# Performance work log

Measured on AMD Instinct MI355X. Metric: run time of the kernel, lower is better.

The kernel has to match this reference:

```python
import jax, jax.numpy as jnp
import numpy as np
import math

H = 256
N = 100000

def setup_inputs() -> dict:
    key = jax.random.key(0)
    ks = jax.random.split(key, 8)
    def xavier(k, shape):
        fan_in, fan_out = shape
        bound = math.sqrt(6.0 / (fan_in + fan_out))
        return jax.random.uniform(k, shape, jnp.float32, -bound, bound)
    return {
        "x": jax.random.normal(ks[0], (N, H), jnp.float32),
        "vec": jax.random.normal(ks[1], (N, 3, H), jnp.float32),
        "node_frame": jax.random.normal(ks[2], (N, 3, 3), jnp.float32),
        # weights stored [in, out]
        "W_equi": xavier(ks[3], (H, 2 * H)),
        "W1": xavier(ks[4], (2 * H, H)),
        "b1": jnp.zeros((H,), jnp.float32),
        "W2": xavier(ks[5], (H, 3 * H)),
        "b2": jnp.zeros((3 * H,), jnp.float32),
    }

def reference(x, vec, node_frame, W_equi, W1, b1, W2, b2):
    inv_sqrt_2 = 1.0 / math.sqrt(2.0)
    inv_sqrt_h = 1.0 / math.sqrt(H)
    # equivariant projection: [N,3,H] @ [H,2H] -> [N,3,2H]
    v = jnp.einsum('nch,hk->nck', vec, W_equi)
    vec1, vec2 = v[..., :H], v[..., H:]
    # scalarization (dead in original output path; scalar below is what is used)
    scalar = jnp.linalg.norm(vec1, axis=-2)          # [N,H], norm over spatial dim
    vec_dot = jnp.sum(vec1 * vec2, axis=1) * inv_sqrt_h  # [N,H]
    h = jnp.concatenate([x, scalar], axis=-1)        # [N,2H]
    h = jax.nn.silu(h @ W1 + b1)                     # [N,H]
    x_vec_h = h @ W2 + b2                            # [N,3H]
    xvec1, xvec2, xvec3 = x_vec_h[:, :H], x_vec_h[:, H:2*H], x_vec_h[:, 2*H:]
    dx = (xvec1 + xvec2 + vec_dot) * inv_sqrt_2      # [N,H]
    dvec = xvec3[:, None, :] * vec2                  # [N,3,H]
    return (dx, dvec)
```

## Files before the change

kernel.cpp:

```cpp
#include <hip/hip_runtime.h>
#include <math.h>

#define H 256
#define R 4

__global__ __launch_bounds__(256) void fte_kernel(
    const float* __restrict__ x,
    const float* __restrict__ vec,
    const float* __restrict__ W_equi,
    const float* __restrict__ W1,
    const float* __restrict__ b1,
    const float* __restrict__ W2,
    const float* __restrict__ b2,
    float* __restrict__ dx,
    float* __restrict__ dvec,
    int N)
{
    __shared__ float vec_s[3 * R * H];
    __shared__ float v1_s[3 * R * H];
    __shared__ float v2_s[3 * R * H];
    __shared__ float hin_s[R * 2 * H];
    __shared__ float h_s[R * H];

    const int t = threadIdx.x;
    const int row0 = blockIdx.x * R;

    {
        const int valid = (N - row0) < R ? (N - row0) : R;
        const int total = valid * 3 * H;
        const float* src = vec + (size_t)row0 * 3 * H;
        if (total == 3 * R * H) {
            const float4* s4 = (const float4*)src;
            float4* d4 = (float4*)vec_s;
            #pragma unroll
            for (int i = 0; i < 3; ++i) d4[t + 256 * i] = s4[t + 256 * i];
        } else {
            for (int i = t; i < total; i += 256) vec_s[i] = src[i];
            for (int i = total + t; i < 3 * R * H; i += 256) vec_s[i] = 0.f;
        }
    }
    __syncthreads();

    float acc0[3 * R], acc1[3 * R];
    #pragma unroll
    for (int m = 0; m < 3 * R; ++m) { acc0[m] = 0.f; acc1[m] = 0.f; }
    for (int h = 0; h < H; h += 4) {
        float w0[4], w1[4];
        #pragma unroll
        for (int u = 0; u < 4; ++u) {
            const float2 w = *(const float2*)&W_equi[(size_t)(h + u) * 2 * H + 2 * t];
            w0[u] = w.x;
            w1[u] = w.y;
        }
        #pragma unroll
        for (int m = 0; m < 3 * R; ++m) {
            const float4 a = *(const float4*)&vec_s[m * H + h];
            acc0[m] += a.x * w0[0]; acc1[m] += a.x * w1[0];
            acc0[m] += a.y * w0[1]; acc1[m] += a.y * w1[1];
            acc0[m] += a.z * w0[2]; acc1[m] += a.z * w1[2];
            acc0[m] += a.w * w0[3]; acc1[m] += a.w * w1[3];
        }
    }
    {
        float* dst = (t < 128) ? v1_s : v2_s;
        const int kk = (2 * t) & (H - 1);
        #pragma unroll
        for (int m = 0; m < 3 * R; ++m) {
            float2 p; p.x = acc0[m]; p.y = acc1[m];
            *(float2*)&dst[m * H + kk] = p;
        }
    }
    __syncthreads();

    float vd[R];
    #pragma unroll
    for (int r = 0; r < R; ++r) {
        float s = 0.f, d = 0.f;
        #pragma unroll
        for (int c = 0; c < 3; ++c) {
            const float a = v1_s[(r * 3 + c) * H + t];
            const float b = v2_s[(r * 3 + c) * H + t];
            s += a * a;
            d += a * b;
        }
        vd[r] = d * (1.0f / 16.0f);
        hin_s[r * 2 * H + H + t] = sqrtf(s);
        float xv = 0.f;
        if (row0 + r < N) xv = x[(size_t)(row0 + r) * H + t];
        hin_s[r * 2 * H + t] = xv;
    }
    __syncthreads();

    float acc2[R];
    #pragma unroll
    for (int r = 0; r < R; ++r) acc2[r] = 0.f;
    for (int k = 0; k < 2 * H; k += 4) {
        float w[4];
        #pragma unroll
        for (int u = 0; u < 4; ++u) w[u] = W1[(size_t)(k + u) * H + t];
        #pragma unroll
        for (int r = 0; r < R; ++r) {
            const float4 a = *(const float4*)&hin_s[r * 2 * H + k];
            acc2[r] += a.x * w[0];
            acc2[r] += a.y * w[1];
            acc2[r] += a.z * w[2];
            acc2[r] += a.w * w[3];
        }
    }
    {
        const float bv = b1[t];
        #pragma unroll
        for (int r = 0; r < R; ++r) {
            const float z = acc2[r] + bv;
            h_s[r * H + t] = z / (1.f + __expf(-z));
        }
    }
    __syncthreads();

    float a3[R][3];
    #pragma unroll
    for (int r = 0; r < R; ++r)
        #pragma unroll
        for (int c = 0; c < 3; ++c) a3[r][c] = 0.f;
    for (int k = 0; k < H; k += 4) {
        float wc[4][3];
        #pragma unroll
        for (int u = 0; u < 4; ++u) {
            const float* wr = W2 + (size_t)(k + u) * 3 * H + t;
            wc[u][0] = wr[0];
            wc[u][1] = wr[H];
            wc[u][2] = wr[2 * H];
        }
        #pragma unroll
        for (int r = 0; r < R; ++r) {
            const float4 a = *(const float4*)&h_s[r * H + k];
            #pragma unroll
            for (int c = 0; c < 3; ++c) {
                a3[r][c] += a.x * wc[0][c];
                a3[r][c] += a.y * wc[1][c];
                a3[r][c] += a.z * wc[2][c];
                a3[r][c] += a.w * wc[3][c];
            }
        }
    }

    const float bv0 = b2[t];
    const float bv1 = b2[H + t];
    const float bv2 = b2[2 * H + t];
    const float inv_sqrt2 = 0.70710678118654752440f;
    #pragma unroll
    for (int r = 0; r < R; ++r) {
        const int n = row0 + r;
        if (n >= N) break;
        const float xv1 = a3[r][0] + bv0;
        const float xv2 = a3[r][1] + bv1;
        const float xv3 = a3[r][2] + bv2;
        dx[(size_t)n * H + t] = (xv1 + xv2 + vd[r]) * inv_sqrt2;
        #pragma unroll
        for (int c = 0; c < 3; ++c) {
            dvec[(size_t)n * 3 * H + c * H + t] = xv3 * v2_s[(r * 3 + c) * H + t];
        }
    }
}

extern "C" void kernel_launch(void* const* d_in, const int* in_sizes, int n_in,
                              void* d_out, int out_size, void* d_ws, size_t ws_size,
                              hipStream_t stream) {
    const float* x      = (const float*)d_in[0];
    const float* vec    = (const float*)d_in[1];
    const float* W_equi = (const float*)d_in[3];
    const float* W1     = (const float*)d_in[4];
    const float* b1     = (const float*)d_in[5];
    const float* W2     = (const float*)d_in[6];
    const float* b2     = (const float*)d_in[7];

    const int N = in_sizes[0] / H;
    float* dx   = (float*)d_out;
    float* dvec = (float*)d_out + (size_t)N * H;

    const int blocks = (N + R - 1) / R;
    fte_kernel<<<blocks, 256, 0, stream>>>(x, vec, W_equi, W1, b1, W2, b2, dx, dvec, N);
}
```

Before: 3.110 ms.

## Process 8 rows per block split into two thread groups with register-resident projections

Doubles rows per block to 8 and splits the 256 threads into two groups of 128, each handling 4 rows and two output columns per thread, so every weight load feeds more FMAs. The equivariant projection results stay in registers for the norm, dot product and dvec output instead of round-tripping through shared memory. A single reused shared buffer replaces the five separate arrays, and outputs use nontemporal stores. The cost is higher register pressure (launch bounds request 4 blocks per SM) and fewer blocks in the grid.

New measurement: 2.538 ms. -18.4%, faster.

```diff
diff --git a/kernel.cpp b/kernel.cpp
--- a/kernel.cpp
+++ b/kernel.cpp
@@ -2,9 +2,12 @@
 #include <math.h>
 
 #define H 256
-#define R 4
-
-__global__ __launch_bounds__(256) void fte_kernel(
+#define R 8
+#define RG 4
+#define AM (3*R)
+#define AMG (3*RG)
+
+__global__ __launch_bounds__(256, 4) void fte_kernel(
     const float* __restrict__ x,
     const float* __restrict__ vec,
     const float* __restrict__ W_equi,
@@ -16,149 +19,190 @@
     float* __restrict__ dvec,
     int N)
 {
-    __shared__ float vec_s[3 * R * H];
-    __shared__ float v1_s[3 * R * H];
-    __shared__ float v2_s[3 * R * H];
-    __shared__ float hin_s[R * 2 * H];
-    __shared__ float h_s[R * H];
-
-    const int t = threadIdx.x;
+    __shared__ float smem[AM * H];
+
+    const int t  = threadIdx.x;
+    const int g  = t >> 7;
+    const int tl = t & 127;
     const int row0 = blockIdx.x * R;
 
     {
-        const int valid = (N - row0) < R ? (N - row0) : R;
-        const int total = valid * 3 * H;
+        const int rem  = N - row0;
+        const int rows = rem < R ? rem : R;
+        const int total = rows * 3 * H;
         const float* src = vec + (size_t)row0 * 3 * H;
-        if (total == 3 * R * H) {
+        if (total == AM * H) {
             const float4* s4 = (const float4*)src;
-            float4* d4 = (float4*)vec_s;
-            #pragma unroll
-            for (int i = 0; i < 3; ++i) d4[t + 256 * i] = s4[t + 256 * i];
+            float4* d4 = (float4*)smem;
+            #pragma unroll
+            for (int i = 0; i < 6; ++i) d4[t + 256 * i] = s4[t + 256 * i];
         } else {
-            for (int i = t; i < total; i += 256) vec_s[i] = src[i];
-            for (int i = total + t; i < 3 * R * H; i += 256) vec_s[i] = 0.f;
-        }
-    }
-    __syncthreads();
-
-    float acc0[3 * R], acc1[3 * R];
-    #pragma unroll
-    for (int m = 0; m < 3 * R; ++m) { acc0[m] = 0.f; acc1[m] = 0.f; }
-    for (int h = 0; h < H; h += 4) {
-        float w0[4], w1[4];
+            for (int i = t; i < total; i += 256) smem[i] = src[i];
+            for (int i = total + t; i < AM * H; i += 256) smem[i] = 0.f;
+        }
+    }
+    __syncthreads();
+
+    float a1[AMG][2], a2[AMG][2];
+    #pragma unroll
+    for (int m = 0; m < AMG; ++m) {
+        a1[m][0] = a1[m][1] = a2[m][0] = a2[m][1] = 0.f;
+    }
+    {
+        const float* As = smem + AMG * H * g;
+        const float* wbase = W_equi + tl;
+        for (int k = 0; k < H; k += 4) {
+            float w[4][4];
+            #pragma unroll
+            for (int u = 0; u < 4; ++u) {
+                const float* wr = wbase + (size_t)(k + u) * (2 * H);
+                w[u][0] = wr[0];
+                w[u][1] = wr[128];
+                w[u][2] = wr[256];
+                w[u][3] = wr[384];
+            }
+            #pragma unroll
+            for (int m = 0; m < AMG; ++m) {
+                const float4 av = *(const float4*)&As[m * H + k];
+                const float aa[4] = {av.x, av.y, av.z, av.w};
+                #pragma unroll
+                for (int u = 0; u < 4; ++u) {
+                    a1[m][0] = fmaf(aa[u], w[u][0], a1[m][0]);
+                    a1[m][1] = fmaf(aa[u], w[u][1], a1[m][1]);
+                    a2[m][0] = fmaf(aa[u], w[u][2], a2[m][0]);
+                    a2[m][1] = fmaf(aa[u], w[u][3], a2[m][1]);
+                }
+            }
+        }
+    }
+
+    float sc[RG][2], vd[RG][2];
+    #pragma unroll
+    for (int nl = 0; nl < RG; ++nl) {
         #pragma unroll
-        for (int u = 0; u < 4; ++u) {
-            const float2 w = *(const float2*)&W_equi[(size_t)(h + u) * 2 * H + 2 * t];
-            w0[u] = w.x;
-            w1[u] = w.y;
-        }
+        for (int jj = 0; jj < 2; ++jj) {
+            float s = 0.f, d = 0.f;
+            #pragma unroll
+            for (int c = 0; c < 3; ++c) {
+                const float u1 = a1[nl * 3 + c][jj];
+                s = fmaf(u1, u1, s);
+                d = fmaf(u1, a2[nl * 3 + c][jj], d);
+            }
+            sc[nl][jj] = sqrtf(s);
+            vd[nl][jj] = d * 0.0625f;
+        }
+    }
+    __syncthreads();
+
+    #pragma unroll
+    for (int nl = 0; nl < RG; ++nl) {
+        smem[(4 * g + nl) * (2 * H) + H + tl]       = sc[nl][0];
+        smem[(4 * g + nl) * (2 * H) + H + tl + 128] = sc[nl][1];
+    }
+    for (int i = t; i < R * (H / 4); i += 256) {
+        const int nb = i >> 6;
+        const int kq = i & 63;
+        const int n = row0 + nb;
+        float4 v = make_float4(0.f, 0.f, 0.f, 0.f);
+        if (n < N) v = ((const float4*)x)[(size_t)n * (H / 4) + kq];
+        *(float4*)&smem[nb * (2 * H) + kq * 4] = v;
+    }
+    __syncthreads();
+
+    float h2[RG][2];
+    #pragma unroll
+    for (int nl = 0; nl < RG; ++nl) { h2[nl][0] = h2[nl][1] = 0.f; }
+    {
+        const float* wbase = W1 + tl;
+        for (int k = 0; k < 2 * H; k += 4) {
+            float w[4][2];
+            #pragma unroll
+            for (int u = 0; u < 4; ++u) {
+                const float* wr = wbase + (size_t)(k + u) * H;
+                w[u][0] = wr[0];
+                w[u][1] = wr[128];
+            }
+            #pragma unroll
+            for (int nl = 0; nl < RG; ++nl) {
+                const float4 av = *(const float4*)&smem[(4 * g + nl) * (2 * H) + k];
+                const float aa[4] = {av.x, av.y, av.z, av.w};
+                #pragma unroll
+                for (int u = 0; u < 4; ++u) {
+                    h2[nl][0] = fmaf(aa[u], w[u][0], h2[nl][0]);
+                    h2[nl][1] = fmaf(aa[u], w[u][1], h2[nl][1]);
+                }
+            }
+        }
+    }
+    {
+        const float bv0 = b1[tl];
+        const float bv1 = b1[tl + 128];
         #pragma unroll
-        for (int m = 0; m < 3 * R; ++m) {
-            const float4 a = *(const float4*)&vec_s[m * H + h];
-            acc0[m] += a.x * w0[0]; acc1[m] += a.x * w1[0];
-            acc0[m] += a.y * w0[1]; acc1[m] += a.y * w1[1];
-            acc0[m] += a.z * w0[2]; acc1[m] += a.z * w1[2];
-            acc0[m] += a.w * w0[3]; acc1[m] += a.w * w1[3];
-        }
-    }
-    {
-        float* dst = (t < 128) ? v1_s : v2_s;
-        const int kk = (2 * t) & (H - 1);
+        for (int nl = 0; nl < RG; ++nl) {
+            const float z0 = h2[nl][0] + bv0;
+            const float z1 = h2[nl][1] + bv1;
+            smem[R * 2 * H + (4 * g + nl) * H + tl]       = z0 / (1.f + __expf(-z0));
+            smem[R * 2 * H + (4 * g + nl) * H + tl + 128] = z1 / (1.f + __expf(-z1));
+        }
+    }
+    __syncthreads();
+
+    float a3[RG][2][3];
+    #pragma unroll
+    for (int nl = 0; nl < RG; ++nl)
         #pragma unroll
-        for (int m = 0; m < 3 * R; ++m) {
-            float2 p; p.x = acc0[m]; p.y = acc1[m];
-            *(float2*)&dst[m * H + kk] = p;
-        }
-    }
-    __syncthreads();
-
-    float vd[R];
-    #pragma unroll
-    for (int r = 0; r < R; ++r) {
-        float s = 0.f, d = 0.f;
-        #pragma unroll
-        for (int c = 0; c < 3; ++c) {
-            const float a = v1_s[(r * 3 + c) * H + t];
-            const float b = v2_s[(r * 3 + c) * H + t];
-            s += a * a;
-            d += a * b;
-        }
-        vd[r] = d * (1.0f / 16.0f);
-        hin_s[r * 2 * H + H + t] = sqrtf(s);
-        float xv = 0.f;
-        if (row0 + r < N) xv = x[(size_t)(row0 + r) * H + t];
-        hin_s[r * 2 * H + t] = xv;
-    }
-    __syncthreads();
-
-    float acc2[R];
-    #pragma unroll
-    for (int r = 0; r < R; ++r) acc2[r] = 0.f;
-    for (int k = 0; k < 2 * H; k += 4) {
-        float w[4];
-        #pragma unroll
-        for (int u = 0; u < 4; ++u) w[u] = W1[(size_t)(k + u) * H + t];
-        #pragma unroll
-        for (int r = 0; r < R; ++r) {
-            const float4 a = *(const float4*)&hin_s[r * 2 * H + k];
-            acc2[r] += a.x * w[0];
-            acc2[r] += a.y * w[1];
-            acc2[r] += a.z * w[2];
-            acc2[r] += a.w * w[3];
-        }
-    }
-    {
-        const float bv = b1[t];
-        #pragma unroll
-        for (int r = 0; r < R; ++r) {
-            const float z = acc2[r] + bv;
-            h_s[r * H + t] = z / (1.f + __expf(-z));
-        }
-    }
-    __syncthreads();
-
-    float a3[R][3];
-    #pragma unroll
-    for (int r = 0; r < R; ++r)
-        #pragma unroll
-        for (int c = 0; c < 3; ++c) a3[r][c] = 0.f;
-    for (int k = 0; k < H; k += 4) {
-        float wc[4][3];
-        #pragma unroll
-        for (int u = 0; u < 4; ++u) {
-            const float* wr = W2 + (size_t)(k + u) * 3 * H + t;
-            wc[u][0] = wr[0];
-            wc[u][1] = wr[H];
-            wc[u][2] = wr[2 * H];
-        }
-        #pragma unroll
-        for (int r = 0; r < R; ++r) {
-            const float4 a = *(const float4*)&h_s[r * H + k];
-            #pragma unroll
-            for (int c = 0; c < 3; ++c) {
-                a3[r][c] += a.x * wc[0][c];
-                a3[r][c] += a.y * wc[1][c];
-                a3[r][c] += a.z * wc[2][c];
-                a3[r][c] += a.w * wc[3][c];
-            }
-        }
-    }
-
-    const float bv0 = b2[t];
-    const float bv1 = b2[H + t];
-    const float bv2 = b2[2 * H + t];
-    const float inv_sqrt2 = 0.70710678118654752440f;
-    #pragma unroll
-    for (int r = 0; r < R; ++r) {
-        const int n = row0 + r;
-        if (n >= N) break;
-        const float xv1 = a3[r][0] + bv0;
-        const float xv2 = a3[r][1] + bv1;
-        const float xv3 = a3[r][2] + bv2;
-        dx[(size_t)n * H + t] = (xv1 + xv2 + vd[r]) * inv_sqrt2;
-        #pragma unroll
-        for (int c = 0; c < 3; ++c) {
-            dvec[(size_t)n * 3 * H + c * H + t] = xv3 * v2_s[(r * 3 + c) * H + t];
+        for (int jj = 0; jj < 2; ++jj)
+            a3[nl][jj][0] = a3[nl][jj][1] = a3[nl][jj][2] = 0.f;
+    {
+        const float* wbase = W2 + tl;
+        for (int k = 0; k < H; k += 4) {
+            float w[4][2][3];
+            #pragma unroll
+            for (int u = 0; u < 4; ++u) {
+                const float* wr = wbase + (size_t)(k + u) * (3 * H);
+                w[u][0][0] = wr[0];       w[u][0][1] = wr[H];       w[u][0][2] = wr[2 * H];
+                w[u][1][0] = wr[128];     w[u][1][1] = wr[H + 128]; w[u][1][2] = wr[2 * H + 128];
+            }
+            #pragma unroll
+            for (int nl = 0; nl < RG; ++nl) {
+                const float4 av = *(const float4*)&smem[R * 2 * H + (4 * g + nl) * H + k];
+                const float aa[4] = {av.x, av.y, av.z, av.w};
+                #pragma unroll
+                for (int u = 0; u < 4; ++u) {
+                    #pragma unroll
+                    for (int jj = 0; jj < 2; ++jj) {
+                        a3[nl][jj][0] = fmaf(aa[u], w[u][jj][0], a3[nl][jj][0]);
+                        a3[nl][jj][1] = fmaf(aa[u], w[u][jj][1], a3[nl][jj][1]);
+                        a3[nl][jj][2] = fmaf(aa[u], w[u][jj][2], a3[nl][jj][2]);
+                    }
+                }
+            }
+        }
+    }
+
+    const float iv2 = 0.70710678118654752440f;
+    const float b2v[2][3] = {
+        {b2[tl],       b2[H + tl],       b2[2 * H + tl]},
+        {b2[tl + 128], b2[H + tl + 128], b2[2 * H + tl + 128]}
+    };
+    #pragma unroll
+    for (int nl = 0; nl < RG; ++nl) {
+        const int n = row0 + 4 * g + nl;
+        if (n < N) {
+            #pragma unroll
+            for (int jj = 0; jj < 2; ++jj) {
+                const int j = tl + 128 * jj;
+                const float xv1 = a3[nl][jj][0] + b2v[jj][0];
+                const float xv2 = a3[nl][jj][1] + b2v[jj][1];
+                const float xv3 = a3[nl][jj][2] + b2v[jj][2];
+                __builtin_nontemporal_store((xv1 + xv2 + vd[nl][jj]) * iv2,
+                                            &dx[(size_t)n * H + j]);
+                #pragma unroll
+                for (int c = 0; c < 3; ++c) {
+                    __builtin_nontemporal_store(xv3 * a2[nl * 3 + c][jj],
+                                                &dvec[((size_t)n * 3 + c) * H + j]);
+                }
+            }
         }
     }
 }
```
